# Kernel optimization log

Hardware: AMD Instinct MI355X
Metric: run time of the kernel (lower is better)

## Reference

```python
import jax, jax.numpy as jnp
import numpy as np

INPUT_DIM = 2048
NUM_EXPERTS = 64
TOP_K = 2


def setup_inputs() -> dict:
    key = jax.random.key(0)
    kx, kw = jax.random.split(key)
    x = jax.random.normal(kx, (4, 4096, INPUT_DIM), dtype=jnp.float32)
    # nn.Linear weight has shape [num_experts, input_dim]
    W = jax.random.normal(kw, (NUM_EXPERTS, INPUT_DIM), dtype=jnp.float32) * (INPUT_DIM ** -0.5)
    return {"x": x, "W": W}


def reference(x, W):
    # Flatten tokens: [N, D]
    x_flat = x.reshape(-1, INPUT_DIM)
    # Gate logits: [N, E]
    gate_logits = jnp.einsum("nd,ed->ne", x_flat, W)
    # Top-k (sorted descending, matching torch.topk)
    top_k_logits, top_k_indices = jax.lax.top_k(gate_logits, TOP_K)
    top_k_values = jax.nn.softmax(top_k_logits, axis=-1)
    return (top_k_indices, top_k_values)
```

## Files before the change

### kernel.cpp

```cpp
#include <hip/hip_runtime.h>
#include <hip/hip_bf16.h>
#include <math.h>

typedef float f4 __attribute__((ext_vector_type(4)));
typedef float f32x4 __attribute__((ext_vector_type(4)));
typedef short bf16x8 __attribute__((ext_vector_type(8)));

#define D      2048
#define NE     64
#define TOKB   32
#define KSPLIT 8
#define KRNG   (D / KSPLIT)
#define KCH    32
#define NCH    (KRNG / KCH)
#define LROW   40
#define SLAB   10240
#define CSTR   68

__device__ __forceinline__ unsigned short bf16rne(float f) {
    unsigned int u = __builtin_bit_cast(unsigned int, f);
    u += 0x7fffu + ((u >> 16) & 1u);
    return (unsigned short)(u >> 16);
}
__device__ __forceinline__ float bf2f(unsigned short h) {
    unsigned int u = (unsigned int)h << 16;
    return __builtin_bit_cast(float, u);
}

__global__ __launch_bounds__(256)
void wprep(const float* __restrict__ W,
           unsigned short* __restrict__ Wh,
           unsigned short* __restrict__ Wl)
{
    const int i = blockIdx.x * 256 + threadIdx.x;
    const float w = W[i];
    const unsigned short h = bf16rne(w);
    Wh[i] = h;
    Wl[i] = bf16rne(w - bf2f(h));
}

#define CVTPAIR(F0, F1, HOUT, LOUT) {                                        \
    __hip_bfloat162 hp_ = __float22bfloat162_rn(make_float2((F0), (F1)));    \
    unsigned hu_; __builtin_memcpy(&hu_, &hp_, 4);                           \
    const float h0_ = __builtin_bit_cast(float, hu_ << 16);                  \
    const float h1_ = __builtin_bit_cast(float, hu_ & 0xffff0000u);          \
    __hip_bfloat162 lp_ = __float22bfloat162_rn(                             \
        make_float2((F0) - h0_, (F1) - h1_));                                \
    unsigned lu_; __builtin_memcpy(&lu_, &lp_, 4);                           \
    HOUT = hu_;                                                              \
    LOUT = lu_;                                                              \
}

__global__ __launch_bounds__(512, 4)
void moe_fused(const float* __restrict__ x,
               const unsigned short* __restrict__ Wh,
               const unsigned short* __restrict__ Wl,
               float* __restrict__ out, int ntok)
{
    __shared__ __align__(16) char smem[KSPLIT][SLAB];

    const int t    = threadIdx.x;
    const int w    = t >> 6;
    const int l    = t & 63;
    const int tok0 = blockIdx.x * TOKB;
    const int k0   = w * KRNG;

    unsigned short* stg = (unsigned short*)smem[w];

    const int srow = l >> 3;
    const int sg   = l & 7;
    const int ar   = l & 15;
    const int akb  = (l >> 4) * 8;
    const int be   = l & 15;

    const float* xbase = x + (size_t)tok0 * D + k0 + sg * 4;

    f4 xr0, xr1, xr2, xr3;

#define LOADX(ch) { \
    const float* p_ = xbase + (ch) * KCH; \
    xr0 = *(const f4*)(p_ + (size_t)(srow     ) * D); \
    xr1 = *(const f4*)(p_ + (size_t)(srow +  8) * D); \
    xr2 = *(const f4*)(p_ + (size_t)(srow + 16) * D); \
    xr3 = *(const f4*)(p_ + (size_t)(srow + 24) * D); }

#define CVT1(v, buf, row) { \
    uint2 hw_, lw_; \
    CVTPAIR(v.x, v.y, hw_.x, lw_.x); \
    CVTPAIR(v.z, v.w, hw_.y, lw_.y); \
    *(uint2*)&stg[(((buf)*2 + 0)*TOKB + (row))*LROW + sg*4] = hw_; \
    *(uint2*)&stg[(((buf)*2 + 1)*TOKB + (row))*LROW + sg*4] = lw_; }

#define CVTWR(buf) { CVT1(xr0, buf, srow); CVT1(xr1, buf, srow+8); \
                     CVT1(xr2, buf, srow+16); CVT1(xr3, buf, srow+24); }

    const f32x4 zz = {0.f, 0.f, 0.f, 0.f};
    f32x4 acc[2][4];
#pragma unroll
    for (int i = 0; i < 2; ++i)
#pragma unroll
        for (int j = 0; j < 4; ++j) acc[i][j] = zz;

    LOADX(0);
    CVTWR(0);

    for (int ch = 0; ch < NCH; ++ch) {
        bf16x8 bh[4], bl[4];
        const size_t kk = (size_t)(k0 + ch * KCH + akb);
#pragma unroll
        for (int et = 0; et < 4; ++et) {
            const size_t off = (size_t)(et * 16 + be) * D + kk;
            bh[et] = *(const bf16x8*)(Wh + off);
            bl[et] = *(const bf16x8*)(Wl + off);
        }
        if (ch + 1 < NCH) LOADX(ch + 1);

        bf16x8 ah[2], al[2];
        const int buf = ch & 1;
#pragma unroll
        for (int rt = 0; rt < 2; ++rt) {
            const int row = rt * 16 + ar;
            ah[rt] = *(const bf16x8*)&stg[((buf*2 + 0)*TOKB + row)*LROW + akb];
            al[rt] = *(const bf16x8*)&stg[((buf*2 + 1)*TOKB + row)*LROW + akb];
        }

#pragma unroll
        for (int rt = 0; rt < 2; ++rt)
#pragma unroll
            for (int et = 0; et < 4; ++et) {
                acc[rt][et] = __builtin_amdgcn_mfma_f32_16x16x32_bf16(ah[rt], bh[et], acc[rt][et], 0, 0, 0);
                acc[rt][et] = __builtin_amdgcn_mfma_f32_16x16x32_bf16(ah[rt], bl[et], acc[rt][et], 0, 0, 0);
                acc[rt][et] = __builtin_amdgcn_mfma_f32_16x16x32_bf16(al[rt], bh[et], acc[rt][et], 0, 0, 0);
            }

        if (ch + 1 < NCH) CVTWR((ch + 1) & 1);
    }

#undef LOADX
#undef CVT1
#undef CVTWR

    float* cred = (float*)smem[w];
#pragma unroll
    for (int rt = 0; rt < 2; ++rt)
#pragma unroll
        for (int et = 0; et < 4; ++et)
#pragma unroll
            for (int r = 0; r < 4; ++r) {
                const int tokl = rt * 16 + (l >> 4) * 4 + r;
                cred[tokl * CSTR + et * 16 + (l & 15)] = acc[rt][et][r];
            }
    __syncthreads();

    if (t < TOKB * 8) {
        const int tokl = t >> 3;
        const int eg   = t & 7;
        f4 s0 = {0.f,0.f,0.f,0.f}, s1 = {0.f,0.f,0.f,0.f};
#pragma unroll
        for (int ww = 0; ww < KSPLIT; ++ww) {
            const float* cw = (const float*)smem[ww] + tokl * CSTR + eg * 8;
            s0 += *(const f4*)cw;
            s1 += *(const f4*)(cw + 4);
        }
        const float vv[8] = {s0.x, s0.y, s0.z, s0.w, s1.x, s1.y, s1.z, s1.w};
        float m1 = -INFINITY, m2 = -INFINITY;
        int i1 = 0, i2 = 0;
#pragma unroll
        for (int j = 0; j < 8; ++j) {
            const float v = vv[j];
            const int id = eg * 8 + j;
            if (v > m1)      { m2 = m1; i2 = i1; m1 = v; i1 = id; }
            else if (v > m2) { m2 = v;  i2 = id; }
        }
#pragma unroll
        for (int m = 1; m < 8; m <<= 1) {
            const float om1 = __shfl_xor(m1, m);
            const int   oi1 = __shfl_xor(i1, m);
            const float om2 = __shfl_xor(m2, m);
            const int   oi2 = __shfl_xor(i2, m);
            const bool b1 = (om1 > m1) || (om1 == m1 && oi1 < i1);
            const float c2v = b1 ? m1 : om1;  const int c2i = b1 ? i1 : oi1;
            const float c3v = b1 ? om2 : m2;  const int c3i = b1 ? oi2 : i2;
            if (b1) { m1 = om1; i1 = oi1; }
            const bool b2 = (c3v > c2v) || (c3v == c2v && c3i < c2i);
            m2 = b2 ? c3v : c2v;  i2 = b2 ? c3i : c2i;
        }
        if (eg == 0) {
            const int tok = tok0 + tokl;
            out[(size_t)tok * 2 + 0] = (float)i1;
            out[(size_t)tok * 2 + 1] = (float)i2;
            const float p1 = 1.0f / (1.0f + expf(m2 - m1));
            float* vals = out + (size_t)ntok * 2;
            vals[(size_t)tok * 2 + 0] = p1;
            vals[(size_t)tok * 2 + 1] = 1.0f - p1;
        }
    }
}

extern "C" void kernel_launch(void* const* d_in, const int* in_sizes, int n_in,
                              void* d_out, int out_size, void* d_ws, size_t ws_size,
                              hipStream_t stream)
{
    const float* x = (const float*)d_in[0];
    const float* W = (const float*)d_in[1];
    float* out = (float*)d_out;
    unsigned short* Wh = (unsigned short*)d_ws;
    unsigned short* Wl = Wh + (size_t)NE * D;

    const int ntok = in_sizes[0] / D;
    wprep<<<(NE * D) / 256, 256, 0, stream>>>(W, Wh, Wl);
    moe_fused<<<ntok / TOKB, 512, 0, stream>>>(x, Wh, Wl, out, ntok);
}
```

Baseline: 48.48 us.

## Prepack W into MFMA fragment order and halve token tile with deeper x prefetch

The weight prep kernel now writes the bf16 hi/lo weights in the exact per-lane fragment order the MFMA loop consumes, so each lane's B loads become contiguous 16-byte reads. The token tile drops from 32 to 16, which doubles the number of blocks and halves LDS per block. The chunk loop is fully unrolled with two-deep register prefetch of x. The smaller tile means each weight load is reused across half as many tokens, so total weight traffic through cache doubles.

```diff
diff --git a/kernel.cpp b/kernel.cpp
--- a/kernel.cpp
+++ b/kernel.cpp
@@ -8,13 +8,13 @@
 
 #define D      2048
 #define NE     64
-#define TOKB   32
+#define TOKB   16
 #define KSPLIT 8
 #define KRNG   (D / KSPLIT)
 #define KCH    32
 #define NCH    (KRNG / KCH)
 #define LROW   40
-#define SLAB   10240
+#define SLAB   5120
 #define CSTR   68
 
 __device__ __forceinline__ unsigned short bf16rne(float f) {
@@ -29,14 +29,20 @@
 
 __global__ __launch_bounds__(256)
 void wprep(const float* __restrict__ W,
-           unsigned short* __restrict__ Wh,
-           unsigned short* __restrict__ Wl)
+           unsigned short* __restrict__ Whp,
+           unsigned short* __restrict__ Wlp)
 {
-    const int i = blockIdx.x * 256 + threadIdx.x;
-    const float w = W[i];
+    const int i  = blockIdx.x * 256 + threadIdx.x;
+    const int j  = i & 7;
+    const int l  = (i >> 3) & 63;
+    const int et = (i >> 9) & 3;
+    const int kc = i >> 11;
+    const int e  = et * 16 + (l & 15);
+    const int k  = kc * 32 + (l >> 4) * 8 + j;
+    const float w = W[(size_t)e * D + k];
     const unsigned short h = bf16rne(w);
-    Wh[i] = h;
-    Wl[i] = bf16rne(w - bf2f(h));
+    Whp[i] = h;
+    Wlp[i] = bf16rne(w - bf2f(h));
 }
 
 #define CVTPAIR(F0, F1, HOUT, LOUT) {                                        \
@@ -53,8 +59,8 @@
 
 __global__ __launch_bounds__(512, 4)
 void moe_fused(const float* __restrict__ x,
-               const unsigned short* __restrict__ Wh,
-               const unsigned short* __restrict__ Wl,
+               const unsigned short* __restrict__ Whp,
+               const unsigned short* __restrict__ Wlp,
                float* __restrict__ out, int ntok)
 {
     __shared__ __align__(16) char smem[KSPLIT][SLAB];
@@ -71,18 +77,15 @@
     const int sg   = l & 7;
     const int ar   = l & 15;
     const int akb  = (l >> 4) * 8;
-    const int be   = l & 15;
 
     const float* xbase = x + (size_t)tok0 * D + k0 + sg * 4;
-
-    f4 xr0, xr1, xr2, xr3;
-
-#define LOADX(ch) { \
+    const unsigned short* whp = Whp + (size_t)w * 16384 + l * 8;
+    const unsigned short* wlp = Wlp + (size_t)w * 16384 + l * 8;
+
+#define LOADX(ch, R0, R1) { \
     const float* p_ = xbase + (ch) * KCH; \
-    xr0 = *(const f4*)(p_ + (size_t)(srow     ) * D); \
-    xr1 = *(const f4*)(p_ + (size_t)(srow +  8) * D); \
-    xr2 = *(const f4*)(p_ + (size_t)(srow + 16) * D); \
-    xr3 = *(const f4*)(p_ + (size_t)(srow + 24) * D); }
+    R0 = *(const f4*)(p_ + (size_t)(srow    ) * D); \
+    R1 = *(const f4*)(p_ + (size_t)(srow + 8) * D); }
 
 #define CVT1(v, buf, row) { \
     uint2 hw_, lw_; \
@@ -91,65 +94,58 @@
     *(uint2*)&stg[(((buf)*2 + 0)*TOKB + (row))*LROW + sg*4] = hw_; \
     *(uint2*)&stg[(((buf)*2 + 1)*TOKB + (row))*LROW + sg*4] = lw_; }
 
-#define CVTWR(buf) { CVT1(xr0, buf, srow); CVT1(xr1, buf, srow+8); \
-                     CVT1(xr2, buf, srow+16); CVT1(xr3, buf, srow+24); }
+#define CVTWR(buf, R0, R1) { CVT1(R0, buf, srow); CVT1(R1, buf, srow + 8); }
+
+#define CHUNK(ch, buf) { \
+    bf16x8 bh[4], bl[4]; \
+    _Pragma("unroll") \
+    for (int et = 0; et < 4; ++et) { \
+        const size_t o_ = (size_t)(4 * (ch) + et) * 512; \
+        bh[et] = *(const bf16x8*)(whp + o_); \
+        bl[et] = *(const bf16x8*)(wlp + o_); \
+    } \
+    const bf16x8 ah = *(const bf16x8*)&stg[(((buf)*2 + 0)*TOKB + ar)*LROW + akb]; \
+    const bf16x8 al = *(const bf16x8*)&stg[(((buf)*2 + 1)*TOKB + ar)*LROW + akb]; \
+    _Pragma("unroll") \
+    for (int et = 0; et < 4; ++et) { \
+        acc[et] = __builtin_amdgcn_mfma_f32_16x16x32_bf16(ah, bh[et], acc[et], 0, 0, 0); \
+        acc[et] = __builtin_amdgcn_mfma_f32_16x16x32_bf16(ah, bl[et], acc[et], 0, 0, 0); \
+        acc[et] = __builtin_amdgcn_mfma_f32_16x16x32_bf16(al, bh[et], acc[et], 0, 0, 0); \
+    } }
 
     const f32x4 zz = {0.f, 0.f, 0.f, 0.f};
-    f32x4 acc[2][4];
-#pragma unroll
-    for (int i = 0; i < 2; ++i)
-#pragma unroll
-        for (int j = 0; j < 4; ++j) acc[i][j] = zz;
-
-    LOADX(0);
-    CVTWR(0);
-
-    for (int ch = 0; ch < NCH; ++ch) {
-        bf16x8 bh[4], bl[4];
-        const size_t kk = (size_t)(k0 + ch * KCH + akb);
-#pragma unroll
-        for (int et = 0; et < 4; ++et) {
-            const size_t off = (size_t)(et * 16 + be) * D + kk;
-            bh[et] = *(const bf16x8*)(Wh + off);
-            bl[et] = *(const bf16x8*)(Wl + off);
-        }
-        if (ch + 1 < NCH) LOADX(ch + 1);
-
-        bf16x8 ah[2], al[2];
-        const int buf = ch & 1;
-#pragma unroll
-        for (int rt = 0; rt < 2; ++rt) {
-            const int row = rt * 16 + ar;
-            ah[rt] = *(const bf16x8*)&stg[((buf*2 + 0)*TOKB + row)*LROW + akb];
-            al[rt] = *(const bf16x8*)&stg[((buf*2 + 1)*TOKB + row)*LROW + akb];
-        }
-
-#pragma unroll
-        for (int rt = 0; rt < 2; ++rt)
-#pragma unroll
-            for (int et = 0; et < 4; ++et) {
-                acc[rt][et] = __builtin_amdgcn_mfma_f32_16x16x32_bf16(ah[rt], bh[et], acc[rt][et], 0, 0, 0);
-                acc[rt][et] = __builtin_amdgcn_mfma_f32_16x16x32_bf16(ah[rt], bl[et], acc[rt][et], 0, 0, 0);
-                acc[rt][et] = __builtin_amdgcn_mfma_f32_16x16x32_bf16(al[rt], bh[et], acc[rt][et], 0, 0, 0);
-            }
-
-        if (ch + 1 < NCH) CVTWR((ch + 1) & 1);
+    f32x4 acc[4] = {zz, zz, zz, zz};
+
+    f4 xE0, xE1, xO0, xO1;
+
+    LOADX(0, xE0, xE1);
+    LOADX(1, xO0, xO1);
+    CVTWR(0, xE0, xE1);
+    LOADX(2, xE0, xE1);
+
+#pragma unroll
+    for (int ch = 0; ch < NCH; ch += 2) {
+        CHUNK(ch, 0);
+        CVTWR(1, xO0, xO1);
+        if (ch + 3 < NCH) LOADX(ch + 3, xO0, xO1);
+        CHUNK(ch + 1, 1);
+        if (ch + 2 < NCH) CVTWR(0, xE0, xE1);
+        if (ch + 4 < NCH) LOADX(ch + 4, xE0, xE1);
     }
 
 #undef LOADX
 #undef CVT1
 #undef CVTWR
+#undef CHUNK
 
     float* cred = (float*)smem[w];
 #pragma unroll
-    for (int rt = 0; rt < 2; ++rt)
-#pragma unroll
-        for (int et = 0; et < 4; ++et)
-#pragma unroll
-            for (int r = 0; r < 4; ++r) {
-                const int tokl = rt * 16 + (l >> 4) * 4 + r;
-                cred[tokl * CSTR + et * 16 + (l & 15)] = acc[rt][et][r];
-            }
+    for (int et = 0; et < 4; ++et)
+#pragma unroll
+        for (int r = 0; r < 4; ++r) {
+            const int tokl = (l >> 4) * 4 + r;
+            cred[tokl * CSTR + et * 16 + (l & 15)] = acc[et][r];
+        }
     __syncthreads();
 
     if (t < TOKB * 8) {
@@ -204,10 +200,10 @@
     const float* x = (const float*)d_in[0];
     const float* W = (const float*)d_in[1];
     float* out = (float*)d_out;
-    unsigned short* Wh = (unsigned short*)d_ws;
-    unsigned short* Wl = Wh + (size_t)NE * D;
+    unsigned short* Whp = (unsigned short*)d_ws;
+    unsigned short* Wlp = Whp + (size_t)NE * D;
 
     const int ntok = in_sizes[0] / D;
-    wprep<<<(NE * D) / 256, 256, 0, stream>>>(W, Wh, Wl);
-    moe_fused<<<ntok / TOKB, 512, 0, stream>>>(x, Wh, Wl, out, ntok);
-}
+    wprep<<<(NE * D) / 256, 256, 0, stream>>>(W, Whp, Wlp);
+    moe_fused<<<ntok / TOKB, 512, 0, stream>>>(x, Whp, Wlp, out, ntok);
+}
```

New measurement: 41.68 us. -14.0%, faster.
